# Kernel tuning notes

Hardware: AMD Instinct MI355X
Metric: run time of the kernel (lower is better)

Reference implementation:

```python
import jax, jax.numpy as jnp
import numpy as np
import math

N_HEADS = 16
EMBED = 1024
D_HEAD = EMBED // N_HEADS
B, L = 2, 2048


def setup_inputs() -> dict:
    key = jax.random.key(0)
    k1, k2, k3, k4, k5 = jax.random.split(key, 5)
    s = 0.02
    return {
        "x": jax.random.normal(k1, (B, L, EMBED), dtype=jnp.float32),
        "w_qkv": jax.random.normal(k2, (3 * EMBED, EMBED), dtype=jnp.float32) * s,
        "b_qkv": jax.random.normal(k3, (3 * EMBED,), dtype=jnp.float32) * s,
        "w_out": jax.random.normal(k4, (EMBED, EMBED), dtype=jnp.float32) * s,
        "b_out": jax.random.normal(k5, (EMBED,), dtype=jnp.float32) * s,
        "mask": 1,
    }


def reference(x, w_qkv, b_qkv, w_out, b_out, mask):
    b, l, e = x.shape
    qkv = x @ w_qkv.T + b_qkv                      # (B, L, 3E)
    q, k, v = jnp.split(qkv, 3, axis=-1)
    # (B, L, H, d) -> (B, H, L, d)
    q = q.reshape(b, l, N_HEADS, D_HEAD).transpose(0, 2, 1, 3)
    k = k.reshape(b, l, N_HEADS, D_HEAD).transpose(0, 2, 1, 3)
    v = v.reshape(b, l, N_HEADS, D_HEAD).transpose(0, 2, 1, 3)
    # NOTE: faithful to source bug -- scores use V, not K
    scores = jnp.einsum("bhld,bhmd->bhlm", q, v) * (1.0 / math.sqrt(D_HEAD))
    if mask:
        causal = jnp.triu(jnp.ones((l, l), dtype=bool), k=1)  # (L, L)
        scores = jnp.where(causal, -jnp.inf, scores)
    attn = jax.nn.softmax(scores, axis=-1)          # (B, H, L, L)
    out = jnp.einsum("bhlm,bhmd->bhld", attn, v)    # (B, H, L, d)
    # NOTE: faithful to source bug -- transpose(1,2) result discarded,
    # so reshape straight from (B, H, L, d) to (B, L, E)
    out = out.reshape(b, l, e)
    return out @ w_out.T + b_out
```

## Files before the change

### kernel.cpp

```cpp
#include <hip/hip_runtime.h>
#include <math.h>

constexpr int Lc = 2048, Ec = 1024, Hc = 16, Dc = 64;

typedef __attribute__((ext_vector_type(8))) short bf16x8;
typedef __attribute__((ext_vector_type(4))) short bf16x4;
typedef __attribute__((ext_vector_type(4))) float f32x4;
typedef unsigned short u16;
typedef unsigned int u32;

#define MFMA32(a, b, c) __builtin_amdgcn_mfma_f32_16x16x32_bf16(a, b, c, 0, 0, 0)

__device__ inline f32x4 mfma_k16(bf16x4 a, bf16x4 b, f32x4 c) {
#if __has_builtin(__builtin_amdgcn_mfma_f32_16x16x16bf16_1k)
  return __builtin_amdgcn_mfma_f32_16x16x16bf16_1k(a, b, c, 0, 0, 0);
#else
  asm("v_mfma_f32_16x16x16_bf16 %0, %1, %2, %0" : "+v"(c) : "v"(a), "v"(b));
  return c;
#endif
}

__device__ inline u16 f2bf(float f) {
  u32 u = __builtin_bit_cast(u32, f);
  u32 r = u + 0x7fff + ((u >> 16) & 1);
  return (u16)(r >> 16);
}

__device__ inline void gld16(const void* g, void* l) {
  __builtin_amdgcn_global_load_lds(
      (const __attribute__((address_space(1))) u32*)g,
      (__attribute__((address_space(3))) u32*)l, 16, 0, 0);
}

constexpr size_t XN = (size_t)4096 * 1024;
constexpr size_t WQN = (size_t)2048 * 1024;
constexpr size_t WON = (size_t)1024 * 1024;

__global__ __launch_bounds__(256) void convert_all(
    const float* __restrict__ x, const float* __restrict__ wqkv,
    const float* __restrict__ wout, u16* __restrict__ xb,
    u16* __restrict__ wqb, u16* __restrict__ wob)
{
  const size_t i = ((size_t)blockIdx.x * 256 + threadIdx.x) * 4;
  float4 v;
  u16* dst;
  if (i < XN) {
    v = *(const float4*)(x + i);
    dst = xb + i;
  } else if (i < XN + WQN) {
    const size_t off = i - XN;
    const size_t row = off >> 10, col = off & 1023;
    const size_t srow = row + ((row >> 10) << 10);
    v = *(const float4*)(wqkv + srow * 1024 + col);
    dst = wqb + off;
  } else {
    const size_t off = i - XN - WQN;
    v = *(const float4*)(wout + off);
    dst = wob + off;
  }
  u16 o0 = f2bf(v.x), o1 = f2bf(v.y), o2 = f2bf(v.z), o3 = f2bf(v.w);
  dst[0] = o0; dst[1] = o1; dst[2] = o2; dst[3] = o3;
}

__global__ __launch_bounds__(256) void gemm_qv(
    const u16* __restrict__ A, const u16* __restrict__ W,
    const float* __restrict__ bqkv, u16* __restrict__ Q, u16* __restrict__ V,
    u16* __restrict__ VT)
{
  __shared__ u16 As[128 * 32];
  __shared__ u16 Bs[128 * 32];
  const int tid = threadIdx.x;
  const int w = tid >> 6, lane = tid & 63;
  const int quad = lane >> 4, l16 = lane & 15;
  const int wm = w >> 1, wn = w & 1;
  const int rowTile = blockIdx.y * 128;
  const int colTile = blockIdx.x * 128;

  const int r0 = tid >> 2, o0 = (tid & 3) * 8;
  const u16* Ab0 = A + (size_t)(rowTile + r0) * 1024 + o0;
  const u16* Ab1 = A + (size_t)(rowTile + r0 + 64) * 1024 + o0;
  const u16* Bb0 = W + (size_t)(colTile + r0) * 1024 + o0;
  const u16* Bb1 = W + (size_t)(colTile + r0 + 64) * 1024 + o0;
  u16* lA0 = &As[(size_t)tid * 8];
  u16* lA1 = &As[(size_t)(tid + 256) * 8];
  u16* lB0 = &Bs[(size_t)tid * 8];
  u16* lB1 = &Bs[(size_t)(tid + 256) * 8];

  f32x4 acc[4][4] = {};

  for (int k0 = 0; k0 < 1024; k0 += 32) {
    __syncthreads();
    gld16(Ab0 + k0, lA0);
    gld16(Ab1 + k0, lA1);
    gld16(Bb0 + k0, lB0);
    gld16(Bb1 + k0, lB1);
    __syncthreads();
    bf16x8 af[4], bf[4];
#pragma unroll
    for (int s = 0; s < 4; ++s)
      af[s] = *(const bf16x8*)&As[(wm * 64 + s * 16 + l16) * 32 + quad * 8];
#pragma unroll
    for (int n = 0; n < 4; ++n)
      bf[n] = *(const bf16x8*)&Bs[(wn * 64 + n * 16 + l16) * 32 + quad * 8];
#pragma unroll
    for (int s = 0; s < 4; ++s)
#pragma unroll
      for (int n = 0; n < 4; ++n)
        acc[s][n] = MFMA32(af[s], bf[n], acc[s][n]);
  }

  const bool isV = (colTile >= 1024);
#pragma unroll
  for (int n = 0; n < 4; ++n) {
    const int gn = colTile + wn * 64 + n * 16 + l16;
    const float bias = bqkv[gn + (isV ? 1024 : 0)];
    const float scl = isV ? 1.0f : 0.125f;
    const int h = (gn & 1023) >> 6, d = gn & 63;
    u16* dst = isV ? V : Q;
#pragma unroll
    for (int s = 0; s < 4; ++s) {
#pragma unroll
      for (int r = 0; r < 4; ++r) {
        const int gm = rowTile + wm * 64 + s * 16 + quad * 4 + r;
        const int b = gm >> 11, l = gm & 2047;
        const u16 val = f2bf((acc[s][n][r] + bias) * scl);
        const size_t bhh = (size_t)(b * Hc + h);
        dst[(bhh * Lc + l) * Dc + d] = val;
        if (isV) VT[(bhh * Dc + d) * Lc + l] = val;
      }
    }
  }
}

constexpr int VTSTR = 68;

__global__ __launch_bounds__(256, 2) void attn_mfma(
    const u16* __restrict__ Q, const u16* __restrict__ V,
    const u16* __restrict__ VT, u16* __restrict__ outA)
{
  __shared__ u16 VsT[64 * VTSTR];
  const int tid = threadIdx.x;
  const int w = tid >> 6, lane = tid & 63;
  const int quad = lane >> 4, l16 = lane & 15;
  const int qt = 15 - (int)blockIdx.x;
  const int q0 = qt * 128;
  const int bh = blockIdx.y;
  const int b = bh >> 4, h = bh & 15;
  const u16* Qb = Q + (size_t)bh * Lc * Dc;
  const u16* Vb = V + (size_t)bh * Lc * Dc;
  const u16* VTb = VT + (size_t)bh * Dc * Lc;
  const int wq0 = q0 + w * 32;
  const int nt = 2 * qt + 2;

  bf16x8 qf[2][2];
#pragma unroll
  for (int s = 0; s < 2; ++s)
#pragma unroll
    for (int kk = 0; kk < 2; ++kk)
      qf[s][kk] = *(const bf16x8*)(Qb + (size_t)(wq0 + s * 16 + l16) * 64 + kk * 32 + quad * 8);

  f32x4 O[4][2] = {};
  float lsum[2] = {0.f, 0.f};

  const int sd = tid >> 2, sk = (tid & 3) * 16;
  bf16x8 stg0 = *(const bf16x8*)(VTb + (size_t)sd * Lc + sk);
  bf16x8 stg1 = *(const bf16x8*)(VTb + (size_t)sd * Lc + sk + 8);
  bf16x8 av[4][2];
#pragma unroll
  for (int nb = 0; nb < 4; ++nb)
#pragma unroll
    for (int kk = 0; kk < 2; ++kk)
      av[nb][kk] = *(const bf16x8*)(Vb + (size_t)(nb * 16 + l16) * 64 + kk * 32 + quad * 8);

  for (int t = 0; t < nt; ++t) {
    const int kt = t * 64;
    __syncthreads();
    *(bf16x8*)&VsT[sd * VTSTR + sk] = stg0;
    *(bf16x8*)&VsT[sd * VTSTR + sk + 8] = stg1;
    if (t + 1 < nt) {
      stg0 = *(const bf16x8*)(VTb + (size_t)sd * Lc + kt + 64 + sk);
      stg1 = *(const bf16x8*)(VTb + (size_t)sd * Lc + kt + 64 + sk + 8);
    }
    __syncthreads();
    if (kt > wq0 + 31) continue;

    f32x4 sf[2][4] = {};
#pragma unroll
    for (int s = 0; s < 2; ++s)
#pragma unroll
      for (int nb = 0; nb < 4; ++nb) {
        sf[s][nb] = MFMA32(av[nb][0], qf[s][0], sf[s][nb]);
        sf[s][nb] = MFMA32(av[nb][1], qf[s][1], sf[s][nb]);
      }
    if (kt + 64 <= wq0 + 31) {
#pragma unroll
      for (int nb = 0; nb < 4; ++nb)
#pragma unroll
        for (int kk = 0; kk < 2; ++kk)
          av[nb][kk] = *(const bf16x8*)(Vb + (size_t)(kt + 64 + nb * 16 + l16) * 64 + kk * 32 + quad * 8);
    }

    bf16x4 vt[4][4];
#pragma unroll
    for (int nb = 0; nb < 4; ++nb)
#pragma unroll
      for (int db = 0; db < 4; ++db)
        vt[nb][db] = *(const bf16x4*)&VsT[(db * 16 + l16) * VTSTR + nb * 16 + quad * 4];

    const bool needmask = (kt + 63 > wq0);
#pragma unroll
    for (int s = 0; s < 2; ++s) {
      bf16x4 pp[4];
#pragma unroll
      for (int nb = 0; nb < 4; ++nb) {
        float p[4];
#pragma unroll
        for (int r = 0; r < 4; ++r) {
          float pv = __expf(sf[s][nb][r]);
          if (needmask && (kt + nb * 16 + quad * 4 + r > wq0 + s * 16 + l16)) pv = 0.f;
          p[r] = pv;
          lsum[s] += pv;
        }
        pp[nb] = (bf16x4){(short)f2bf(p[0]), (short)f2bf(p[1]),
                          (short)f2bf(p[2]), (short)f2bf(p[3])};
      }
#pragma unroll
      for (int nb = 0; nb < 4; ++nb)
#pragma unroll
        for (int db = 0; db < 4; ++db)
          O[db][s] = mfma_k16(vt[nb][db], pp[nb], O[db][s]);
    }
  }

#pragma unroll
  for (int s = 0; s < 2; ++s) {
    float l = lsum[s];
    l += __shfl_xor(l, 16);
    l += __shfl_xor(l, 32);
    const float inv = 1.f / l;
    const int q = wq0 + s * 16 + l16;
    const int row = h * 128 + (q >> 4);
    const size_t base = ((size_t)b * Lc + row) * Ec + ((q & 15) << 6);
#pragma unroll
    for (int db = 0; db < 4; ++db) {
      const u32 lo = (u32)f2bf(O[db][s][0] * inv) | ((u32)f2bf(O[db][s][1] * inv) << 16);
      const u32 hi = (u32)f2bf(O[db][s][2] * inv) | ((u32)f2bf(O[db][s][3] * inv) << 16);
      *(uint2*)(outA + base + db * 16 + quad * 4) = make_uint2(lo, hi);
    }
  }
}

__global__ __launch_bounds__(256) void gemm_out(
    const u16* __restrict__ A, const u16* __restrict__ W,
    const float* __restrict__ bias, float* __restrict__ out)
{
  __shared__ u16 As[64 * 32];
  __shared__ u16 Bs[128 * 32];
  const int tid = threadIdx.x;
  const int w = tid >> 6, lane = tid & 63;
  const int quad = lane >> 4, l16 = lane & 15;
  const int wm = w & 1, wn = w >> 1;
  const int rowTile = blockIdx.y * 64;
  const int colTile = blockIdx.x * 128;

  const int r0 = tid >> 2, o0 = (tid & 3) * 8;
  const u16* Ab0 = A + (size_t)(rowTile + r0) * 1024 + o0;
  const u16* Bb0 = W + (size_t)(colTile + r0) * 1024 + o0;
  const u16* Bb1 = W + (size_t)(colTile + r0 + 64) * 1024 + o0;
  u16* lA0 = &As[(size_t)tid * 8];
  u16* lB0 = &Bs[(size_t)tid * 8];
  u16* lB1 = &Bs[(size_t)(tid + 256) * 8];

  f32x4 acc[2][4] = {};

  for (int k0 = 0; k0 < 1024; k0 += 32) {
    __syncthreads();
    gld16(Ab0 + k0, lA0);
    gld16(Bb0 + k0, lB0);
    gld16(Bb1 + k0, lB1);
    __syncthreads();
    bf16x8 af[2], bf[4];
#pragma unroll
    for (int s = 0; s < 2; ++s)
      af[s] = *(const bf16x8*)&As[(wm * 32 + s * 16 + l16) * 32 + quad * 8];
#pragma unroll
    for (int n = 0; n < 4; ++n)
      bf[n] = *(const bf16x8*)&Bs[(wn * 64 + n * 16 + l16) * 32 + quad * 8];
#pragma unroll
    for (int s = 0; s < 2; ++s)
#pragma unroll
      for (int n = 0; n < 4; ++n)
        acc[s][n] = MFMA32(af[s], bf[n], acc[s][n]);
  }

#pragma unroll
  for (int n = 0; n < 4; ++n) {
    const int gn = colTile + wn * 64 + n * 16 + l16;
    const float bn = bias[gn];
#pragma unroll
    for (int s = 0; s < 2; ++s)
#pragma unroll
      for (int r = 0; r < 4; ++r) {
        const int gm = rowTile + wm * 32 + s * 16 + quad * 4 + r;
        out[(size_t)gm * 1024 + gn] = acc[s][n][r] + bn;
      }
  }
}

extern "C" void kernel_launch(void* const* d_in, const int* in_sizes, int n_in,
                              void* d_out, int out_size, void* d_ws, size_t ws_size,
                              hipStream_t stream) {
  (void)in_sizes; (void)n_in; (void)out_size; (void)ws_size;
  const float* x     = (const float*)d_in[0];
  const float* w_qkv = (const float*)d_in[1];
  const float* b_qkv = (const float*)d_in[2];
  const float* w_out = (const float*)d_in[3];
  const float* b_out = (const float*)d_in[4];
  float* out = (float*)d_out;

  constexpr size_t QVN = (size_t)2 * Hc * Lc * Dc;
  u16* xb  = (u16*)d_ws;
  u16* wqb = xb + XN;
  u16* wob = wqb + WQN;
  u16* Qw  = wob + WON;
  u16* Vw  = Qw + QVN;
  u16* VTw = Vw + QVN;
  u16* Aw  = VTw + QVN;

  convert_all<<<7168, 256, 0, stream>>>(x, w_qkv, w_out, xb, wqb, wob);
  gemm_qv<<<dim3(16, 32), 256, 0, stream>>>(xb, wqb, b_qkv, Qw, Vw, VTw);
  attn_mfma<<<dim3(16, 32), 256, 0, stream>>>(Qw, Vw, VTw, Aw);
  gemm_out<<<dim3(8, 64), 256, 0, stream>>>(Aw, wob, b_out, out);
}
```

Before: 209.3 us.

## Drop LDS staging of V^T in attention; load per-wave from global

The attention kernel no longer stages the transposed V tile in shared memory with block-wide barriers. Each wave now loads V and V^T fragments straight from global memory and runs only as many key tiles as its own causal range needs. The occupancy hint rises from 2 to 3 blocks per SM, and the bf16 packing now uses a perm-based round-half-up instead of round-to-nearest-even. This removes the __syncthreads and the cases where waves idle through tiles they skip. In exchange it loses the software prefetch, issues strided uncoalesced global loads for V^T, and changes rounding slightly.

```diff
diff --git a/kernel.cpp b/kernel.cpp
--- a/kernel.cpp
+++ b/kernel.cpp
@@ -6,6 +6,7 @@
 typedef __attribute__((ext_vector_type(8))) short bf16x8;
 typedef __attribute__((ext_vector_type(4))) short bf16x4;
 typedef __attribute__((ext_vector_type(4))) float f32x4;
+typedef __attribute__((ext_vector_type(2))) unsigned int u32x2;
 typedef unsigned short u16;
 typedef unsigned int u32;
 
@@ -24,6 +25,12 @@
   u32 u = __builtin_bit_cast(u32, f);
   u32 r = u + 0x7fff + ((u >> 16) & 1);
   return (u16)(r >> 16);
+}
+
+__device__ inline u32 pack2bf(float a, float b) {
+  const u32 ua = __builtin_bit_cast(u32, a) + 0x8000u;
+  const u32 ub = __builtin_bit_cast(u32, b) + 0x8000u;
+  return __builtin_amdgcn_perm(ub, ua, 0x07060302u);
 }
 
 __device__ inline void gld16(const void* g, void* l) {
@@ -132,13 +139,10 @@
   }
 }
 
-constexpr int VTSTR = 68;
-
-__global__ __launch_bounds__(256, 2) void attn_mfma(
+__global__ __launch_bounds__(256, 3) void attn_mfma(
     const u16* __restrict__ Q, const u16* __restrict__ V,
     const u16* __restrict__ VT, u16* __restrict__ outA)
 {
-  __shared__ u16 VsT[64 * VTSTR];
   const int tid = threadIdx.x;
   const int w = tid >> 6, lane = tid & 63;
   const int quad = lane >> 4, l16 = lane & 15;
@@ -150,7 +154,7 @@
   const u16* Vb = V + (size_t)bh * Lc * Dc;
   const u16* VTb = VT + (size_t)bh * Dc * Lc;
   const int wq0 = q0 + w * 32;
-  const int nt = 2 * qt + 2;
+  const int ntw = ((wq0 + 31) >> 6) + 1;
 
   bf16x8 qf[2][2];
 #pragma unroll
@@ -162,27 +166,21 @@
   f32x4 O[4][2] = {};
   float lsum[2] = {0.f, 0.f};
 
-  const int sd = tid >> 2, sk = (tid & 3) * 16;
-  bf16x8 stg0 = *(const bf16x8*)(VTb + (size_t)sd * Lc + sk);
-  bf16x8 stg1 = *(const bf16x8*)(VTb + (size_t)sd * Lc + sk + 8);
-  bf16x8 av[4][2];
-#pragma unroll
-  for (int nb = 0; nb < 4; ++nb)
-#pragma unroll
-    for (int kk = 0; kk < 2; ++kk)
-      av[nb][kk] = *(const bf16x8*)(Vb + (size_t)(nb * 16 + l16) * 64 + kk * 32 + quad * 8);
-
-  for (int t = 0; t < nt; ++t) {
+  for (int t = 0; t < ntw; ++t) {
     const int kt = t * 64;
-    __syncthreads();
-    *(bf16x8*)&VsT[sd * VTSTR + sk] = stg0;
-    *(bf16x8*)&VsT[sd * VTSTR + sk + 8] = stg1;
-    if (t + 1 < nt) {
-      stg0 = *(const bf16x8*)(VTb + (size_t)sd * Lc + kt + 64 + sk);
-      stg1 = *(const bf16x8*)(VTb + (size_t)sd * Lc + kt + 64 + sk + 8);
-    }
-    __syncthreads();
-    if (kt > wq0 + 31) continue;
+
+    bf16x8 av[4][2];
+#pragma unroll
+    for (int nb = 0; nb < 4; ++nb)
+#pragma unroll
+      for (int kk = 0; kk < 2; ++kk)
+        av[nb][kk] = *(const bf16x8*)(Vb + (size_t)(kt + nb * 16 + l16) * 64 + kk * 32 + quad * 8);
+    bf16x4 vt[4][4];
+#pragma unroll
+    for (int nb = 0; nb < 4; ++nb)
+#pragma unroll
+      for (int db = 0; db < 4; ++db)
+        vt[nb][db] = *(const bf16x4*)(VTb + (size_t)(db * 16 + l16) * Lc + kt + nb * 16 + quad * 4);
 
     f32x4 sf[2][4] = {};
 #pragma unroll
@@ -192,20 +190,6 @@
         sf[s][nb] = MFMA32(av[nb][0], qf[s][0], sf[s][nb]);
         sf[s][nb] = MFMA32(av[nb][1], qf[s][1], sf[s][nb]);
       }
-    if (kt + 64 <= wq0 + 31) {
-#pragma unroll
-      for (int nb = 0; nb < 4; ++nb)
-#pragma unroll
-        for (int kk = 0; kk < 2; ++kk)
-          av[nb][kk] = *(const bf16x8*)(Vb + (size_t)(kt + 64 + nb * 16 + l16) * 64 + kk * 32 + quad * 8);
-    }
-
-    bf16x4 vt[4][4];
-#pragma unroll
-    for (int nb = 0; nb < 4; ++nb)
-#pragma unroll
-      for (int db = 0; db < 4; ++db)
-        vt[nb][db] = *(const bf16x4*)&VsT[(db * 16 + l16) * VTSTR + nb * 16 + quad * 4];
 
     const bool needmask = (kt + 63 > wq0);
 #pragma unroll
@@ -221,8 +205,10 @@
           p[r] = pv;
           lsum[s] += pv;
         }
-        pp[nb] = (bf16x4){(short)f2bf(p[0]), (short)f2bf(p[1]),
-                          (short)f2bf(p[2]), (short)f2bf(p[3])};
+        u32x2 t2;
+        t2.x = pack2bf(p[0], p[1]);
+        t2.y = pack2bf(p[2], p[3]);
+        pp[nb] = __builtin_bit_cast(bf16x4, t2);
       }
 #pragma unroll
       for (int nb = 0; nb < 4; ++nb)
```

Result: slower. 312.6 us (+49.4%).
